# Kernel optimization log

Measured on AMD Instinct MI355X. Metric: run time of the kernel, lower is better.

Reference implementation:

```python
import jax, jax.numpy as jnp
import numpy as np

N_WIRES = 6
DIM = 1 << N_WIRES  # 64, equals input channel dim C for amplitude encoding
HID = N_WIRES       # hidden_dim = len(ops)


def _rx(theta):
    c = jnp.cos(theta / 2).astype(jnp.complex64)
    s = jnp.sin(theta / 2).astype(jnp.complex64)
    return jnp.stack([jnp.stack([c, -1j * s]), jnp.stack([-1j * s, c])])


def _ry(theta):
    c = jnp.cos(theta / 2).astype(jnp.complex64)
    s = jnp.sin(theta / 2).astype(jnp.complex64)
    return jnp.stack([jnp.stack([c, -s]), jnp.stack([s, c])])


def _apply_1q(state, U, wire):
    # state: (N, 2, 2, ..., 2); apply 2x2 U on qubit axis wire+1
    s = jnp.moveaxis(state, wire + 1, 1)
    s = jnp.einsum('ab,nb...->na...', U, s)
    return jnp.moveaxis(s, 1, wire + 1)


def _apply_cnot(state, c, t):
    # flip target axis where control bit == 1
    s = jnp.moveaxis(state, (c + 1, t + 1), (1, 2))
    s = jnp.concatenate([s[:, :1], jnp.flip(s[:, 1:2], axis=2)], axis=1)
    return jnp.moveaxis(s, (1, 2), (c + 1, t + 1))


def _expval_z(state, wire):
    # <Z_wire> = P(bit=0) - P(bit=1)
    p = state.real ** 2 + state.imag ** 2
    p = jnp.moveaxis(p, wire + 1, 1).reshape(p.shape[0], 2, -1)
    return p[:, 0].sum(-1) - p[:, 1].sum(-1)


def _value_layer(x_flat, params, qk):
    # amplitude encoding: normalize input into state amplitudes (C == DIM)
    norm = jnp.linalg.norm(x_flat, axis=-1, keepdims=True)
    psi = (x_flat / norm).astype(jnp.complex64)
    state = psi.reshape((x_flat.shape[0],) + (2,) * N_WIRES)
    rx0, ry0, ry1 = params[0], params[1], params[2]
    for j in range(N_WIRES):
        state = _apply_1q(state, _rx(rx0[j]), j)
        state = _apply_1q(state, _ry(ry0[j]), j)
    for j in range(N_WIRES):
        state = _apply_cnot(state, j, (j + 1) % N_WIRES)
    for j in range(N_WIRES):
        state = _apply_1q(state, _ry(ry1[j]), j)
    if qk:
        z0 = _expval_z(state, 0)
        return jnp.stack([z0] * HID, axis=-1)  # qk=True replicates wire-0 <Z>
    return jnp.stack([_expval_z(state, w) for w in range(N_WIRES)], axis=-1)


def setup_inputs() -> dict:
    key = jax.random.key(0)
    k1, k2, k3, k4 = jax.random.split(key, 4)
    B, T, C = 16, 2048, DIM
    return {
        'x': jax.random.normal(k1, (B, T, C), dtype=jnp.float32),
        'params_q': jax.random.normal(k2, (3, N_WIRES), dtype=jnp.float32),
        'params_k': jax.random.normal(k3, (3, N_WIRES), dtype=jnp.float32),
        'params_v': jax.random.normal(k4, (3, N_WIRES), dtype=jnp.float32),
    }


def reference(x, params_q, params_k, params_v):
    B, T, C = x.shape
    xf = x.reshape(B * T, C)
    q = _value_layer(xf, params_q, True).reshape(B, T, HID)
    k = _value_layer(xf, params_k, True).reshape(B, T, HID)
    v = _value_layer(xf, params_v, False).reshape(B, T, HID)
    scores = jnp.einsum('btd,bsd->bts', q, k) / jnp.sqrt(jnp.float32(HID))
    attn = jax.nn.softmax(scores, axis=-1)
    return jnp.einsum('bts,bsd->btd', attn, v)
```

## Files before the change

### kernel.cpp

```cpp
#include <hip/hip_runtime.h>
#include <math.h>

#define NWIRES 6
#define DIM 64
#define NTOK 32768
#define NBATCH 16
#define TPB 2048
#define NMOM 16
#define SQRT6F 2.4494897427831781f
#define CSTRIDE 160

__global__ void qsa_prep(const float* __restrict__ pq,
                         const float* __restrict__ pk,
                         const float* __restrict__ pv,
                         float* __restrict__ cs) {
    int b = threadIdx.x;
    for (int circ = 0; circ < 3; ++circ) {
        const float* p = (circ == 0) ? pq : (circ == 1 ? pk : pv);
        float* T = cs + circ * CSTRIDE;
        float d = 0.f;
#pragma unroll
        for (int j = 0; j < 6; ++j)
            d += 0.5f * p[j] * ((b & (32 >> j)) ? -1.f : 1.f);
        float sd, cd;
        sincosf(d, &sd, &cd);
        T[b] = cd;
        T[64 + b] = sd;
        if (b < 12) {
            float s, c;
            sincosf(0.5f * p[6 + b], &s, &c);
            T[128 + b * 2 + 0] = c;
            T[128 + b * 2 + 1] = s;
        }
    }
}

template<int M>
__device__ __forceinline__ void whad(float* v) {
#pragma unroll
    for (int i = 0; i < DIM; ++i) {
        if (i & M) continue;
        int j = i | M;
        float a = v[i], b = v[j];
        v[i] = a + b;
        v[j] = a - b;
    }
}

template<int M>
__device__ __forceinline__ void ryr(float* v, float c, float s) {
#pragma unroll
    for (int i = 0; i < DIM; ++i) {
        if (i & M) continue;
        int j = i | M;
        float a = v[i], b = v[j];
        v[i] = c * a - s * b;
        v[j] = s * a + c * b;
    }
}

template<int MC, int MT>
__device__ __forceinline__ void cnr(float* v) {
#pragma unroll
    for (int i = 0; i < DIM; ++i) {
        if (!(i & MC) || (i & MT)) continue;
        int j = i | MT;
        float t = v[i]; v[i] = v[j]; v[j] = t;
    }
}

__global__ __attribute__((amdgpu_waves_per_eu(1, 4)))
__launch_bounds__(256) void qsa_sim(
        const float* __restrict__ x,
        const float* __restrict__ cs,
        float* __restrict__ zq,
        float* __restrict__ kv) {
    int g = blockIdx.x * 256 + threadIdx.x;
    int par = g & 1;
    int token = g >> 1;
    int circ = blockIdx.y;
    const float* T = cs + circ * CSTRIDE;
    const float* P = T + 128;

    float v[DIM];
    const float4* xp4 = (const float4*)(x + (size_t)token * DIM);
#pragma unroll
    for (int k = 0; k < DIM / 4; ++k) {
        float4 q = xp4[k];
        v[4*k+0] = q.x; v[4*k+1] = q.y; v[4*k+2] = q.z; v[4*k+3] = q.w;
    }

    whad<32>(v); whad<16>(v); whad<8>(v); whad<4>(v); whad<2>(v); whad<1>(v);
    const float4* tp4 = (const float4*)(T + par * 64);
#pragma unroll
    for (int k = 0; k < DIM / 4; ++k) {
        float4 q = tp4[k];
        v[4*k+0] *= q.x; v[4*k+1] *= q.y; v[4*k+2] *= q.z; v[4*k+3] *= q.w;
    }
    whad<32>(v); whad<16>(v); whad<8>(v); whad<4>(v); whad<2>(v); whad<1>(v);

    ryr<32>(v, P[0],  P[1]);
    ryr<16>(v, P[2],  P[3]);
    ryr< 8>(v, P[4],  P[5]);
    ryr< 4>(v, P[6],  P[7]);
    ryr< 2>(v, P[8],  P[9]);
    ryr< 1>(v, P[10], P[11]);
    cnr<32,16>(v);
    cnr<16, 8>(v);
    cnr< 8, 4>(v);
    cnr< 4, 2>(v);
    cnr< 2, 1>(v);
    cnr< 1,32>(v);
    ryr<32>(v, P[12], P[13]);
    ryr<16>(v, P[14], P[15]);
    ryr< 8>(v, P[16], P[17]);
    ryr< 4>(v, P[18], P[19]);
    ryr< 2>(v, P[20], P[21]);
    ryr< 1>(v, P[22], P[23]);

    if (circ < 2) {
        float nl = 0.f, s0 = 0.f;
#pragma unroll
        for (int i = 0; i < DIM; ++i) {
            float p2 = v[i] * v[i];
            nl += p2;
            if (!(i & 32)) s0 += p2;
        }
        float norm2 = nl + __shfl_xor(nl, 1, 64);
        float S0 = s0 + __shfl_xor(s0, 1, 64);
        float z0 = (2.f * S0 - norm2) / norm2;
        if (par == 0) {
            if (circ == 0) zq[token] = SQRT6F * z0;
            else           kv[(size_t)token * 8] = z0;
        }
    } else {
        float nl = 0.f, s0=0.f, s1=0.f, s2=0.f, s3=0.f, s4=0.f, s5=0.f;
#pragma unroll
        for (int i = 0; i < DIM; ++i) {
            float p2 = v[i] * v[i];
            nl += p2;
            if (!(i & 32)) s0 += p2;
            if (!(i & 16)) s1 += p2;
            if (!(i &  8)) s2 += p2;
            if (!(i &  4)) s3 += p2;
            if (!(i &  2)) s4 += p2;
            if (!(i &  1)) s5 += p2;
        }
        float norm2 = nl + __shfl_xor(nl, 1, 64);
        float S0 = s0 + __shfl_xor(s0, 1, 64);
        float S1 = s1 + __shfl_xor(s1, 1, 64);
        float S2 = s2 + __shfl_xor(s2, 1, 64);
        float S3 = s3 + __shfl_xor(s3, 1, 64);
        float S4 = s4 + __shfl_xor(s4, 1, 64);
        float S5 = s5 + __shfl_xor(s5, 1, 64);
        float inv = 1.0f / norm2;
        float* o = kv + (size_t)token * 8;
        if (par == 0) {
            o[1] = (2.f*S0 - norm2) * inv;
            o[2] = (2.f*S1 - norm2) * inv;
            o[3] = (2.f*S2 - norm2) * inv;
        } else {
            o[4] = (2.f*S3 - norm2) * inv;
            o[5] = (2.f*S4 - norm2) * inv;
            o[6] = (2.f*S5 - norm2) * inv;
        }
    }
}

__global__ __attribute__((amdgpu_waves_per_eu(1, 2)))
__launch_bounds__(64) void qsa_moments_partial(
        const float* __restrict__ kv,
        float* __restrict__ mpart) {
    int blk = blockIdx.x;
    int b = blk >> 3, c = blk & 7;
    int lane = threadIdx.x;
    float S[NMOM], H[NMOM][6];
#pragma unroll
    for (int m = 0; m < NMOM; ++m) {
        S[m] = 0.f;
#pragma unroll
        for (int w = 0; w < 6; ++w) H[m][w] = 0.f;
    }
    const float* base = kv + ((size_t)(b * TPB + c * 256)) * 8;
#pragma unroll
    for (int r = 0; r < 4; ++r) {
        const float4* e = (const float4*)(base + (size_t)(r * 64 + lane) * 8);
        float4 e0 = e[0], e1 = e[1];
        float z = e0.x;
        float v0 = e0.y, v1 = e0.z, v2 = e0.w, v3 = e1.x, v4 = e1.y, v5 = e1.z;
        float pw = 1.f;
#pragma unroll
        for (int m = 0; m < NMOM; ++m) {
            S[m] += pw;
            H[m][0] += pw * v0; H[m][1] += pw * v1; H[m][2] += pw * v2;
            H[m][3] += pw * v3; H[m][4] += pw * v4; H[m][5] += pw * v5;
            pw *= z;
        }
    }
#pragma unroll
    for (int d = 32; d >= 1; d >>= 1) {
#pragma unroll
        for (int m = 0; m < NMOM; ++m) {
            S[m] += __shfl_xor(S[m], d, 64);
#pragma unroll
            for (int w = 0; w < 6; ++w) H[m][w] += __shfl_xor(H[m][w], d, 64);
        }
    }
    if (lane == 0) {
        float* o = mpart + (size_t)blk * 112;
#pragma unroll
        for (int m = 0; m < NMOM; ++m) {
            float* om = o + m * 7;
            om[0] = S[m];
            om[1] = H[m][0]; om[2] = H[m][1]; om[3] = H[m][2];
            om[4] = H[m][3]; om[5] = H[m][4]; om[6] = H[m][5];
        }
    }
}

__global__ __launch_bounds__(256) void qsa_eval(
        const float* __restrict__ zq,
        const float* __restrict__ mpart,
        float* __restrict__ out) {
    __shared__ float sm[112];
    int bk = blockIdx.x;
    int b = bk >> 3;
    int tid = threadIdx.x;
    if (tid < 112) {
        float s = 0.f;
#pragma unroll
        for (int c = 0; c < 8; ++c) s += mpart[(size_t)(b * 8 + c) * 112 + tid];
        sm[tid] = s;
    }
    __syncthreads();

    int t = bk * 256 + tid;
    float a = zq[t];
    float den = 0.f, o0 = 0.f, o1 = 0.f, o2 = 0.f, o3 = 0.f, o4 = 0.f, o5 = 0.f;
    float pw = 1.f;
#pragma unroll
    for (int m = 0; m < NMOM; ++m) {
        const float* mm = sm + m * 7;
        den += pw * mm[0];
        o0 += pw * mm[1]; o1 += pw * mm[2]; o2 += pw * mm[3];
        o3 += pw * mm[4]; o4 += pw * mm[5]; o5 += pw * mm[6];
        pw *= a * (1.0f / (m + 1));
    }
    float inv = 1.0f / den;
    float* o = out + (size_t)t * 6;
    float2* o2p = (float2*)o;
    o2p[0] = make_float2(o0 * inv, o1 * inv);
    o2p[1] = make_float2(o2 * inv, o3 * inv);
    o2p[2] = make_float2(o4 * inv, o5 * inv);
}

extern "C" void kernel_launch(void* const* d_in, const int* in_sizes, int n_in,
                              void* d_out, int out_size, void* d_ws, size_t ws_size,
                              hipStream_t stream) {
    const float* x  = (const float*)d_in[0];
    const float* pq = (const float*)d_in[1];
    const float* pk = (const float*)d_in[2];
    const float* pv = (const float*)d_in[3];
    float* w = (float*)d_ws;
    float* cs    = w;
    float* zq    = w + 512;
    float* kv    = w + 512 + NTOK;
    float* mpart = w + 512 + NTOK + NTOK * 8;
    float* out   = (float*)d_out;

    qsa_prep<<<1, 64, 0, stream>>>(pq, pk, pv, cs);
    qsa_sim<<<dim3(NTOK * 2 / 256, 3), 256, 0, stream>>>(x, cs, zq, kv);
    qsa_moments_partial<<<NBATCH * 8, 64, 0, stream>>>(kv, mpart);
    qsa_eval<<<NTOK / 256, 256, 0, stream>>>(zq, mpart, out);
}
```

Before: 90.72 us.

## Fold circuit into dense matrices and apply via split-bf16 MFMA

```diff
diff --git a/kernel.cpp b/kernel.cpp
--- a/kernel.cpp
+++ b/kernel.cpp
@@ -9,6 +9,18 @@
 #define NMOM 16
 #define SQRT6F 2.4494897427831781f
 #define CSTRIDE 160
+#define XPAD 72
+
+typedef short bf16x8 __attribute__((ext_vector_type(8)));
+typedef float f32x4  __attribute__((ext_vector_type(4)));
+
+__device__ __forceinline__ unsigned f2bfbits(float f) {
+    unsigned u = __float_as_uint(f);
+    return (u + 0x7FFF + ((u >> 16) & 1)) >> 16;
+}
+__device__ __forceinline__ float bfbits2f(unsigned b) {
+    return __uint_as_float(b << 16);
+}
 
 __global__ void qsa_prep(const float* __restrict__ pq,
                          const float* __restrict__ pk,
@@ -36,18 +48,6 @@
 }
 
 template<int M>
-__device__ __forceinline__ void whad(float* v) {
-#pragma unroll
-    for (int i = 0; i < DIM; ++i) {
-        if (i & M) continue;
-        int j = i | M;
-        float a = v[i], b = v[j];
-        v[i] = a + b;
-        v[j] = a - b;
-    }
-}
-
-template<int M>
 __device__ __forceinline__ void ryr(float* v, float c, float s) {
 #pragma unroll
     for (int i = 0; i < DIM; ++i) {
@@ -58,7 +58,6 @@
         v[j] = s * a + c * b;
     }
 }
-
 template<int MC, int MT>
 __device__ __forceinline__ void cnr(float* v) {
 #pragma unroll
@@ -69,100 +68,162 @@
     }
 }
 
-__global__ __attribute__((amdgpu_waves_per_eu(1, 4)))
+__global__ __attribute__((amdgpu_waves_per_eu(1, 1)))
+__launch_bounds__(64) void qsa_prepM(const float* __restrict__ cs,
+                                     unsigned short* __restrict__ Apack) {
+    int c = blockIdx.x, k = threadIdx.x;
+    const float* T = cs + c * CSTRIDE;
+    const float* P = T + 128;
+    unsigned short* Ah = Apack + (size_t)c * 16384;
+    unsigned short* Al = Ah + 8192;
+    for (int ph = 0; ph < 2; ++ph) {
+        float v[DIM];
+#pragma unroll
+        for (int i = 0; i < DIM; ++i) {
+            float sgn = (__popc(i & k) & 1) ? -1.f : 1.f;
+            v[i] = T[ph * 64 + i] * sgn;
+        }
+#pragma unroll
+        for (int M = 32; M >= 1; M >>= 1) {
+#pragma unroll
+            for (int i = 0; i < DIM; ++i) {
+                if (i & M) continue;
+                int j = i | M;
+                float a = v[i], b = v[j];
+                v[i] = a + b; v[j] = a - b;
+            }
+        }
+        ryr<32>(v, P[0],  P[1]);
+        ryr<16>(v, P[2],  P[3]);
+        ryr< 8>(v, P[4],  P[5]);
+        ryr< 4>(v, P[6],  P[7]);
+        ryr< 2>(v, P[8],  P[9]);
+        ryr< 1>(v, P[10], P[11]);
+        cnr<32,16>(v); cnr<16,8>(v); cnr<8,4>(v);
+        cnr<4,2>(v);   cnr<2,1>(v);  cnr<1,32>(v);
+        ryr<32>(v, P[12], P[13]);
+        ryr<16>(v, P[14], P[15]);
+        ryr< 8>(v, P[16], P[17]);
+        ryr< 4>(v, P[18], P[19]);
+        ryr< 2>(v, P[20], P[21]);
+        ryr< 1>(v, P[22], P[23]);
+#pragma unroll
+        for (int r = 0; r < DIM; ++r) {
+            unsigned hb = f2bfbits(v[r]);
+            unsigned lb = f2bfbits(v[r] - bfbits2f(hb));
+            int row = ph * 64 + r;
+            Ah[row * 64 + k] = (unsigned short)hb;
+            Al[row * 64 + k] = (unsigned short)lb;
+        }
+    }
+}
+
+__global__ __attribute__((amdgpu_waves_per_eu(2, 4)))
 __launch_bounds__(256) void qsa_sim(
         const float* __restrict__ x,
-        const float* __restrict__ cs,
+        const unsigned short* __restrict__ Apack,
         float* __restrict__ zq,
         float* __restrict__ kv) {
-    int g = blockIdx.x * 256 + threadIdx.x;
-    int par = g & 1;
-    int token = g >> 1;
+    __shared__ unsigned short sXh[64 * XPAD];
+    __shared__ unsigned short sXl[64 * XPAD];
+    int tid = threadIdx.x;
+    int tbase = blockIdx.x * 64;
     int circ = blockIdx.y;
-    const float* T = cs + circ * CSTRIDE;
-    const float* P = T + 128;
-
-    float v[DIM];
-    const float4* xp4 = (const float4*)(x + (size_t)token * DIM);
-#pragma unroll
-    for (int k = 0; k < DIM / 4; ++k) {
-        float4 q = xp4[k];
-        v[4*k+0] = q.x; v[4*k+1] = q.y; v[4*k+2] = q.z; v[4*k+3] = q.w;
-    }
-
-    whad<32>(v); whad<16>(v); whad<8>(v); whad<4>(v); whad<2>(v); whad<1>(v);
-    const float4* tp4 = (const float4*)(T + par * 64);
-#pragma unroll
-    for (int k = 0; k < DIM / 4; ++k) {
-        float4 q = tp4[k];
-        v[4*k+0] *= q.x; v[4*k+1] *= q.y; v[4*k+2] *= q.z; v[4*k+3] *= q.w;
-    }
-    whad<32>(v); whad<16>(v); whad<8>(v); whad<4>(v); whad<2>(v); whad<1>(v);
-
-    ryr<32>(v, P[0],  P[1]);
-    ryr<16>(v, P[2],  P[3]);
-    ryr< 8>(v, P[4],  P[5]);
-    ryr< 4>(v, P[6],  P[7]);
-    ryr< 2>(v, P[8],  P[9]);
-    ryr< 1>(v, P[10], P[11]);
-    cnr<32,16>(v);
-    cnr<16, 8>(v);
-    cnr< 8, 4>(v);
-    cnr< 4, 2>(v);
-    cnr< 2, 1>(v);
-    cnr< 1,32>(v);
-    ryr<32>(v, P[12], P[13]);
-    ryr<16>(v, P[14], P[15]);
-    ryr< 8>(v, P[16], P[17]);
-    ryr< 4>(v, P[18], P[19]);
-    ryr< 2>(v, P[20], P[21]);
-    ryr< 1>(v, P[22], P[23]);
-
-    if (circ < 2) {
-        float nl = 0.f, s0 = 0.f;
-#pragma unroll
-        for (int i = 0; i < DIM; ++i) {
-            float p2 = v[i] * v[i];
-            nl += p2;
-            if (!(i & 32)) s0 += p2;
-        }
-        float norm2 = nl + __shfl_xor(nl, 1, 64);
-        float S0 = s0 + __shfl_xor(s0, 1, 64);
-        float z0 = (2.f * S0 - norm2) / norm2;
-        if (par == 0) {
-            if (circ == 0) zq[token] = SQRT6F * z0;
-            else           kv[(size_t)token * 8] = z0;
-        }
-    } else {
-        float nl = 0.f, s0=0.f, s1=0.f, s2=0.f, s3=0.f, s4=0.f, s5=0.f;
-#pragma unroll
-        for (int i = 0; i < DIM; ++i) {
-            float p2 = v[i] * v[i];
-            nl += p2;
-            if (!(i & 32)) s0 += p2;
-            if (!(i & 16)) s1 += p2;
-            if (!(i &  8)) s2 += p2;
-            if (!(i &  4)) s3 += p2;
-            if (!(i &  2)) s4 += p2;
-            if (!(i &  1)) s5 += p2;
-        }
-        float norm2 = nl + __shfl_xor(nl, 1, 64);
-        float S0 = s0 + __shfl_xor(s0, 1, 64);
-        float S1 = s1 + __shfl_xor(s1, 1, 64);
-        float S2 = s2 + __shfl_xor(s2, 1, 64);
-        float S3 = s3 + __shfl_xor(s3, 1, 64);
-        float S4 = s4 + __shfl_xor(s4, 1, 64);
-        float S5 = s5 + __shfl_xor(s5, 1, 64);
-        float inv = 1.0f / norm2;
-        float* o = kv + (size_t)token * 8;
-        if (par == 0) {
-            o[1] = (2.f*S0 - norm2) * inv;
-            o[2] = (2.f*S1 - norm2) * inv;
-            o[3] = (2.f*S2 - norm2) * inv;
+    const unsigned short* Ah = Apack + (size_t)circ * 16384;
+    const unsigned short* Al = Ah + 8192;
+
+#pragma unroll
+    for (int rr = 0; rr < 4; ++rr) {
+        int i = rr * 256 + tid;
+        int tok = i >> 4, ch = i & 15;
+        float4 q = ((const float4*)(x + ((size_t)(tbase + tok)) * 64))[ch];
+        unsigned h0 = f2bfbits(q.x), h1 = f2bfbits(q.y),
+                 h2 = f2bfbits(q.z), h3 = f2bfbits(q.w);
+        unsigned l0 = f2bfbits(q.x - bfbits2f(h0)),
+                 l1 = f2bfbits(q.y - bfbits2f(h1)),
+                 l2 = f2bfbits(q.z - bfbits2f(h2)),
+                 l3 = f2bfbits(q.w - bfbits2f(h3));
+        uint2 hp = make_uint2(h0 | (h1 << 16), h2 | (h3 << 16));
+        uint2 lp = make_uint2(l0 | (l1 << 16), l2 | (l3 << 16));
+        *(uint2*)(&sXh[tok * XPAD + ch * 4]) = hp;
+        *(uint2*)(&sXl[tok * XPAD + ch * 4]) = lp;
+    }
+    __syncthreads();
+
+    int lane = tid & 63, wv = tid >> 6;
+    int q4 = lane >> 4, c16 = lane & 15;
+    int mytok = wv * 16 + c16;
+
+    bf16x8 xh[2], xl[2];
+#pragma unroll
+    for (int ks = 0; ks < 2; ++ks) {
+        int el = mytok * XPAD + ks * 32 + q4 * 8;
+        xh[ks] = *(const bf16x8*)(&sXh[el]);
+        xl[ks] = *(const bf16x8*)(&sXl[el]);
+    }
+
+    f32x4 acc[8];
+#pragma unroll
+    for (int mt = 0; mt < 8; ++mt) acc[mt] = (f32x4){0.f, 0.f, 0.f, 0.f};
+
+#pragma unroll
+    for (int mt = 0; mt < 8; ++mt) {
+        int r = mt * 16 + c16;
+#pragma unroll
+        for (int ks = 0; ks < 2; ++ks) {
+            const bf16x8 ah = *(const bf16x8*)(Ah + r * 64 + ks * 32 + q4 * 8);
+            const bf16x8 al = *(const bf16x8*)(Al + r * 64 + ks * 32 + q4 * 8);
+            acc[mt] = __builtin_amdgcn_mfma_f32_16x16x32_bf16(ah, xh[ks], acc[mt], 0, 0, 0);
+            acc[mt] = __builtin_amdgcn_mfma_f32_16x16x32_bf16(ah, xl[ks], acc[mt], 0, 0, 0);
+            acc[mt] = __builtin_amdgcn_mfma_f32_16x16x32_bf16(al, xh[ks], acc[mt], 0, 0, 0);
+        }
+    }
+
+    float n = 0.f, s0 = 0.f, s1 = 0.f, s2 = 0.f, s3 = 0.f, s4 = 0.f, s5 = 0.f;
+    float f2 = (q4 < 2) ? 1.f : 0.f;
+    float f3 = (q4 & 1) ? 0.f : 1.f;
+#pragma unroll
+    for (int mt = 0; mt < 4; ++mt) {
+#pragma unroll
+        for (int rg = 0; rg < 4; ++rg) {
+            float dc = acc[mt][rg];
+            float ds = acc[mt + 4][rg];
+            float p = dc * dc + ds * ds;
+            n += p;
+            if (!(mt & 2)) s0 += p;
+            if (!(mt & 1)) s1 += p;
+            s2 += f2 * p;
+            s3 += f3 * p;
+            if (!(rg & 2)) s4 += p;
+            if (!(rg & 1)) s5 += p;
+        }
+    }
+#pragma unroll
+    for (int d = 16; d <= 32; d <<= 1) {
+        n  += __shfl_xor(n,  d, 64);
+        s0 += __shfl_xor(s0, d, 64);
+        s1 += __shfl_xor(s1, d, 64);
+        s2 += __shfl_xor(s2, d, 64);
+        s3 += __shfl_xor(s3, d, 64);
+        s4 += __shfl_xor(s4, d, 64);
+        s5 += __shfl_xor(s5, d, 64);
+    }
+    if (q4 == 0) {
+        int t = tbase + mytok;
+        float inv = 1.0f / n;
+        if (circ == 0) {
+            zq[t] = SQRT6F * (2.f * s0 - n) * inv;
+        } else if (circ == 1) {
+            kv[(size_t)t * 8] = (2.f * s0 - n) * inv;
         } else {
-            o[4] = (2.f*S3 - norm2) * inv;
-            o[5] = (2.f*S4 - norm2) * inv;
-            o[6] = (2.f*S5 - norm2) * inv;
+            float* o = kv + (size_t)t * 8;
+            o[1] = (2.f*s0 - n) * inv;
+            o[2] = (2.f*s1 - n) * inv;
+            o[3] = (2.f*s2 - n) * inv;
+            o[4] = (2.f*s3 - n) * inv;
+            o[5] = (2.f*s4 - n) * inv;
+            o[6] = (2.f*s5 - n) * inv;
+            o[7] = 0.f;
         }
     }
 }
@@ -262,14 +323,16 @@
     const float* pk = (const float*)d_in[2];
     const float* pv = (const float*)d_in[3];
     float* w = (float*)d_ws;
-    float* cs    = w;
-    float* zq    = w + 512;
-    float* kv    = w + 512 + NTOK;
-    float* mpart = w + 512 + NTOK + NTOK * 8;
-    float* out   = (float*)d_out;
+    float* cs            = w;
+    unsigned short* Apk  = (unsigned short*)(w + 512);
+    float* zq            = w + 512 + 24576;
+    float* kv            = zq + NTOK;
+    float* mpart         = kv + NTOK * 8;
+    float* out           = (float*)d_out;
 
     qsa_prep<<<1, 64, 0, stream>>>(pq, pk, pv, cs);
-    qsa_sim<<<dim3(NTOK * 2 / 256, 3), 256, 0, stream>>>(x, cs, zq, kv);
+    qsa_prepM<<<3, 64, 0, stream>>>(cs, Apk);
+    qsa_sim<<<dim3(NTOK / 64, 3), 256, 0, stream>>>(x, Apk, zq, kv);
     qsa_moments_partial<<<NBATCH * 8, 64, 0, stream>>>(kv, mpart);
     qsa_eval<<<NTOK / 256, 256, 0, stream>>>(zq, mpart, out);
 }
```

Result: slower. 113.0 us (+24.6%).
